# Kernel tuning notes

Measured on AMD Instinct MI355X. Metric: run time of the kernel, lower is better.

The kernel has to match this reference:

```python
import jax, jax.numpy as jnp
import numpy as np
from jax import lax

B_SZ, L, D, N = 4, 2048, 768, 16


def setup_inputs() -> dict:
    key = jax.random.key(0)
    ks = jax.random.split(key, 8)
    x = jax.random.normal(ks[0], (B_SZ, L, D), dtype=jnp.float32)
    # A_log init: log(repeat(arange(1, N+1), 'n -> d n'))
    A_log = jnp.log(jnp.tile(jnp.arange(1, N + 1, dtype=jnp.float32), (D, 1)))  # (D, N)
    sD = 1.0 / np.sqrt(D)
    Wb = jax.random.normal(ks[1], (N, D), dtype=jnp.float32) * sD
    bb = jax.random.normal(ks[2], (N,), dtype=jnp.float32) * sD
    Wc = jax.random.normal(ks[3], (N, D), dtype=jnp.float32) * sD
    bc = jax.random.normal(ks[4], (N,), dtype=jnp.float32) * sD
    W1 = jax.random.normal(ks[5], (1, D), dtype=jnp.float32) * sD
    b1 = jnp.zeros((1,), dtype=jnp.float32)
    Wd = jax.random.normal(ks[6], (D, 1), dtype=jnp.float32)
    bd = jax.random.normal(ks[7], (D,), dtype=jnp.float32)
    return {"x": x, "A_log": A_log, "Wb": Wb, "bb": bb, "Wc": Wc, "bc": bc,
            "W1": W1, "b1": b1, "Wd": Wd, "bd": bd}


def reference(x, A_log, Wb, bb, Wc, bc, W1, b1, Wd, bd):
    # x: (b, l, d)
    A = -jnp.exp(A_log)                                   # (d, n)
    Bp = x @ Wb.T + bb                                    # (b, l, n)
    C = x @ Wc.T + bc                                     # (b, l, n)
    s1 = x @ W1.T + b1                                    # (b, l, 1)
    delta = jax.nn.softplus(s1 @ Wd.T + bd)               # (b, l, d)
    deltaA = jnp.exp(jnp.einsum('bld,dn->bldn', delta, A))          # (b, l, d, n)
    deltaB_u = jnp.einsum('bld,bln,bld->bldn', delta, Bp, x)        # (b, l, d, n)

    def step(h, inputs):
        dA, dBu, c = inputs                               # (b,d,n),(b,d,n),(b,n)
        h = dA * h + dBu
        y = jnp.einsum('bdn,bn->bd', h, c)
        return h, y

    b, l, d = x.shape
    n = A_log.shape[1]
    h0 = jnp.zeros((b, d, n), dtype=x.dtype)
    _, ys = lax.scan(step, h0, (jnp.moveaxis(deltaA, 1, 0),
                                jnp.moveaxis(deltaB_u, 1, 0),
                                jnp.moveaxis(C, 1, 0)))
    return jnp.moveaxis(ys, 0, 1)                          # (b, l, d)
```

## Files before the change

kernel.cpp:

```cpp
#include <hip/hip_runtime.h>
#include <hip/hip_cooperative_groups.h>
#include <math.h>

namespace cg = cooperative_groups;

#define B_SZ 4
#define LSEQ 2048
#define DDIM 768
#define NST  16
#define NROW (B_SZ * LSEQ)
#define NJ   33

#define NC   64
#define CS   (LSEQ / NC)
#define CPG  (NC / 4)

#define KSPL 16
#define KCH  (DDIM / KSPL)

__global__ __launch_bounds__(256) void proj_part_kernel(
    const float* __restrict__ x,
    const float* __restrict__ Wb, const float* __restrict__ Wc,
    const float* __restrict__ W1, float* __restrict__ part)
{
    const int row = blockIdx.x * 256 + threadIdx.x;
    const int s = blockIdx.y;
    const int k0 = s * KCH;

    float4 xv[KCH / 4];
    const float* xp = x + (size_t)row * DDIM + k0;
    #pragma unroll
    for (int q = 0; q < KCH / 4; ++q) xv[q] = *(const float4*)(xp + q * 4);

    float acc[NJ];
    #pragma unroll
    for (int j = 0; j < NJ; ++j) {
        const float* wrow = (j < 16) ? (Wb + j * DDIM)
                          : (j < 32) ? (Wc + (j - 16) * DDIM)
                                     : W1;
        const float* wk = wrow + k0;
        float a = 0.f;
        #pragma unroll
        for (int q = 0; q < KCH / 4; ++q) {
            a = fmaf(xv[q].x, wk[q * 4 + 0], a);
            a = fmaf(xv[q].y, wk[q * 4 + 1], a);
            a = fmaf(xv[q].z, wk[q * 4 + 2], a);
            a = fmaf(xv[q].w, wk[q * 4 + 3], a);
        }
        acc[j] = a;
    }
    #pragma unroll
    for (int j = 0; j < NJ; ++j)
        part[((size_t)s * NJ + j) * NROW + row] = acc[j];
}

__global__ __launch_bounds__(256) void proj_reduce_kernel(
    const float* __restrict__ part,
    const float* __restrict__ bb, const float* __restrict__ bc,
    const float* __restrict__ b1,
    float* __restrict__ Bp, float* __restrict__ Cc, float* __restrict__ s1)
{
    const int idx = blockIdx.x * 256 + threadIdx.x;
    if (idx >= NJ * NROW) return;
    const int j = idx / NROW;
    const int row = idx % NROW;
    float a = 0.f;
    #pragma unroll
    for (int s = 0; s < KSPL; ++s)
        a += part[((size_t)s * NJ + j) * NROW + row];
    if (j < 16)      Bp[(size_t)row * NST + j] = a + bb[j];
    else if (j < 32) Cc[(size_t)row * NST + (j - 16)] = a + bc[j - 16];
    else             s1[row] = a + b1[0];
}

__device__ __forceinline__ float softplus_f(float z) {
    float t = __expf(-fabsf(z));
    return fmaxf(z, 0.f) + __logf(1.f + t);
}

__device__ __forceinline__ void powers16(float p, float* e) {
    e[0] = p;      e[1] = p * p;      e[2] = e[1] * p;   e[3] = e[1] * e[1];
    e[4] = e[3] * p;  e[5] = e[3] * e[1];  e[6] = e[3] * e[2];  e[7] = e[3] * e[3];
    e[8] = e[7] * p;  e[9] = e[7] * e[1];  e[10] = e[7] * e[2]; e[11] = e[7] * e[3];
    e[12] = e[7] * e[4]; e[13] = e[7] * e[5]; e[14] = e[7] * e[6]; e[15] = e[7] * e[7];
}

__device__ __forceinline__ bool a_structured(const float* acoef) {
    bool st = true;
    #pragma unroll
    for (int n = 0; n < NST; ++n)
        st = st && (fabsf(acoef[n] - (float)(n + 1) * acoef[0]) <= 1e-5f * fabsf(acoef[n]));
    return __all(st) != 0;
}

__device__ __forceinline__ void phaseA_body(
    int b, int c, int d,
    const float* __restrict__ x, const float* __restrict__ Wd, const float* __restrict__ bd,
    const float* __restrict__ Bp, const float* __restrict__ s1,
    const float* acoef, float a0, bool structured,
    float* __restrict__ Ssum, float* __restrict__ Q)
{
    const int rowbase = b * LSEQ + c * CS;
    const float wd = Wd[d], bdv = bd[d];
    const float4* B4 = (const float4*)(Bp + (size_t)rowbase * NST);
    const float* s1p = s1 + rowbase;
    const float* xp = x + (size_t)rowbase * DDIM + d;

    float h[NST];
    #pragma unroll
    for (int n = 0; n < NST; ++n) h[n] = 0.f;
    float S = 0.f;

    if (structured) {
        #pragma unroll 4
        for (int l = 0; l < CS; ++l) {
            const float delta = softplus_f(fmaf(s1p[l], wd, bdv));
            S += delta;
            float e[NST];
            powers16(__expf(delta * a0), e);
            const float dx = delta * xp[(size_t)l * DDIM];
            const float4 b0 = B4[l * 4 + 0], b1v = B4[l * 4 + 1];
            const float4 b2 = B4[l * 4 + 2], b3v = B4[l * 4 + 3];
            const float bv[NST] = {b0.x, b0.y, b0.z, b0.w, b1v.x, b1v.y, b1v.z, b1v.w,
                                   b2.x, b2.y, b2.z, b2.w, b3v.x, b3v.y, b3v.z, b3v.w};
            #pragma unroll
            for (int n = 0; n < NST; ++n) h[n] = fmaf(e[n], h[n], dx * bv[n]);
        }
    } else {
        #pragma unroll 4
        for (int l = 0; l < CS; ++l) {
            const float delta = softplus_f(fmaf(s1p[l], wd, bdv));
            S += delta;
            float e[NST];
            #pragma unroll
            for (int n = 0; n < NST; ++n) e[n] = __expf(delta * acoef[n]);
            const float dx = delta * xp[(size_t)l * DDIM];
            const float4 b0 = B4[l * 4 + 0], b1v = B4[l * 4 + 1];
            const float4 b2 = B4[l * 4 + 2], b3v = B4[l * 4 + 3];
            const float bv[NST] = {b0.x, b0.y, b0.z, b0.w, b1v.x, b1v.y, b1v.z, b1v.w,
                                   b2.x, b2.y, b2.z, b2.w, b3v.x, b3v.y, b3v.z, b3v.w};
            #pragma unroll
            for (int n = 0; n < NST; ++n) h[n] = fmaf(e[n], h[n], dx * bv[n]);
        }
    }
    Ssum[((size_t)b * NC + c) * DDIM + d] = S;
    const size_t gbase = (((size_t)b * NC + c) * DDIM + d) * NST;
    float4* Q4 = (float4*)(Q + gbase);
    #pragma unroll
    for (int q = 0; q < 4; ++q)
        Q4[q] = make_float4(h[q * 4], h[q * 4 + 1], h[q * 4 + 2], h[q * 4 + 3]);
}

__device__ __forceinline__ void phaseB_body(
    int gidx, int lane,
    const float* __restrict__ A_log,
    const float* __restrict__ Ssum, const float* __restrict__ Q,
    float* __restrict__ Hin)
{
    const int rlow = gidx & 15;
    const int g = (gidx >> 4) & 3;
    const int hi = gidx >> 6;
    const int pairIdx = hi * 16 + rlow;
    const int b2 = pairIdx / (DDIM * NST);
    const int r = pairIdx % (DDIM * NST);
    const int d2 = r >> 4;
    const float ac = -__expf(A_log[r]);
    const int c0 = g * CPG;

    float eq[CPG], qq[CPG];
    #pragma unroll
    for (int ci = 0; ci < CPG; ++ci) {
        const size_t base = (size_t)(b2 * NC + c0 + ci);
        eq[ci] = __expf(ac * Ssum[base * DDIM + d2]);
        qq[ci] = Q[base * (DDIM * NST) + r];
    }
    float E = 1.f, H = 0.f;
    #pragma unroll
    for (int ci = 0; ci < CPG; ++ci) { H = fmaf(eq[ci], H, qq[ci]); E *= eq[ci]; }

    float oE = __shfl_up(E, 16, 64);
    float oH = __shfl_up(H, 16, 64);
    if (lane >= 16) { H = fmaf(E, oH, H); E *= oE; }
    oE = __shfl_up(E, 32, 64);
    oH = __shfl_up(H, 32, 64);
    if (lane >= 32) { H = fmaf(E, oH, H); E *= oE; }

    float hin = __shfl_up(H, 16, 64);
    if (g == 0) hin = 0.f;

    float h = hin;
    #pragma unroll
    for (int ci = 0; ci < CPG; ++ci) {
        const size_t base = (size_t)(b2 * NC + c0 + ci);
        Hin[base * (DDIM * NST) + r] = h;
        h = fmaf(eq[ci], h, qq[ci]);
    }
}

__device__ __forceinline__ void phaseC_body(
    int b, int c, int d,
    const float* __restrict__ x, const float* __restrict__ Wd, const float* __restrict__ bd,
    const float* __restrict__ Bp, const float* __restrict__ Cc,
    const float* __restrict__ s1, const float* __restrict__ Hin,
    const float* acoef, float a0, bool structured,
    float* __restrict__ out)
{
    const int rowbase = b * LSEQ + c * CS;
    const float wd = Wd[d], bdv = bd[d];
    const float4* B4 = (const float4*)(Bp + (size_t)rowbase * NST);
    const float4* C4 = (const float4*)(Cc + (size_t)rowbase * NST);
    const float* s1p = s1 + rowbase;
    const float* xp = x + (size_t)rowbase * DDIM + d;
    float* yp = out + (size_t)rowbase * DDIM + d;

    float h[NST];
    const size_t gbase = (((size_t)b * NC + c) * DDIM + d) * NST;
    const float4* H4 = (const float4*)(Hin + gbase);
    #pragma unroll
    for (int q = 0; q < 4; ++q) {
        const float4 hv = H4[q];
        h[q * 4] = hv.x; h[q * 4 + 1] = hv.y; h[q * 4 + 2] = hv.z; h[q * 4 + 3] = hv.w;
    }

    if (structured) {
        #pragma unroll 4
        for (int l = 0; l < CS; ++l) {
            const float delta = softplus_f(fmaf(s1p[l], wd, bdv));
            float e[NST];
            powers16(__expf(delta * a0), e);
            const float dx = delta * xp[(size_t)l * DDIM];
            const float4 b0 = B4[l * 4 + 0], b1v = B4[l * 4 + 1];
            const float4 b2 = B4[l * 4 + 2], b3v = B4[l * 4 + 3];
            const float4 c0v = C4[l * 4 + 0], c1v = C4[l * 4 + 1];
            const float4 c2v = C4[l * 4 + 2], c3v = C4[l * 4 + 3];
            const float bv[NST] = {b0.x, b0.y, b0.z, b0.w, b1v.x, b1v.y, b1v.z, b1v.w,
                                   b2.x, b2.y, b2.z, b2.w, b3v.x, b3v.y, b3v.z, b3v.w};
            const float cv[NST] = {c0v.x, c0v.y, c0v.z, c0v.w, c1v.x, c1v.y, c1v.z, c1v.w,
                                   c2v.x, c2v.y, c2v.z, c2v.w, c3v.x, c3v.y, c3v.z, c3v.w};
            float y = 0.f;
            #pragma unroll
            for (int n = 0; n < NST; ++n) {
                h[n] = fmaf(e[n], h[n], dx * bv[n]);
                y = fmaf(h[n], cv[n], y);
            }
            yp[(size_t)l * DDIM] = y;
        }
    } else {
        #pragma unroll 4
        for (int l = 0; l < CS; ++l) {
            const float delta = softplus_f(fmaf(s1p[l], wd, bdv));
            float e[NST];
            #pragma unroll
            for (int n = 0; n < NST; ++n) e[n] = __expf(delta * acoef[n]);
            const float dx = delta * xp[(size_t)l * DDIM];
            const float4 b0 = B4[l * 4 + 0], b1v = B4[l * 4 + 1];
            const float4 b2 = B4[l * 4 + 2], b3v = B4[l * 4 + 3];
            const float4 c0v = C4[l * 4 + 0], c1v = C4[l * 4 + 1];
            const float4 c2v = C4[l * 4 + 2], c3v = C4[l * 4 + 3];
            const float bv[NST] = {b0.x, b0.y, b0.z, b0.w, b1v.x, b1v.y, b1v.z, b1v.w,
                                   b2.x, b2.y, b2.z, b2.w, b3v.x, b3v.y, b3v.z, b3v.w};
            const float cv[NST] = {c0v.x, c0v.y, c0v.z, c0v.w, c1v.x, c1v.y, c1v.z, c1v.w,
                                   c2v.x, c2v.y, c2v.z, c2v.w, c3v.x, c3v.y, c3v.z, c3v.w};
            float y = 0.f;
            #pragma unroll
            for (int n = 0; n < NST; ++n) {
                h[n] = fmaf(e[n], h[n], dx * bv[n]);
                y = fmaf(h[n], cv[n], y);
            }
            yp[(size_t)l * DDIM] = y;
        }
    }
}

__global__ __launch_bounds__(256) void pass1_kernel(
    const float* __restrict__ x, const float* __restrict__ A_log,
    const float* __restrict__ Wd, const float* __restrict__ bd,
    const float* __restrict__ Bp, const float* __restrict__ s1,
    float* __restrict__ Ssum, float* __restrict__ Q)
{
    const int d = blockIdx.x * 256 + threadIdx.x;
    const int c = blockIdx.y, b = blockIdx.z;
    float acoef[NST];
    #pragma unroll
    for (int n = 0; n < NST; ++n) acoef[n] = -__expf(A_log[d * NST + n]);
    const bool structured = a_structured(acoef);
    phaseA_body(b, c, d, x, Wd, bd, Bp, s1, acoef, acoef[0], structured, Ssum, Q);
}

__global__ __launch_bounds__(256) void combine_kernel(
    const float* __restrict__ A_log,
    const float* __restrict__ Ssum, const float* __restrict__ Q,
    float* __restrict__ Hin)
{
    const int gidx = blockIdx.x * 256 + threadIdx.x;
    phaseB_body(gidx, threadIdx.x & 63, A_log, Ssum, Q, Hin);
}

__global__ __launch_bounds__(256) void pass2_kernel(
    const float* __restrict__ x, const float* __restrict__ A_log,
    const float* __restrict__ Wd, const float* __restrict__ bd,
    const float* __restrict__ Bp, const float* __restrict__ Cc,
    const float* __restrict__ s1, const float* __restrict__ Hin,
    float* __restrict__ out)
{
    const int d = blockIdx.x * 256 + threadIdx.x;
    const int c = blockIdx.y, b = blockIdx.z;
    float acoef[NST];
    #pragma unroll
    for (int n = 0; n < NST; ++n) acoef[n] = -__expf(A_log[d * NST + n]);
    const bool structured = a_structured(acoef);
    phaseC_body(b, c, d, x, Wd, bd, Bp, Cc, s1, Hin, acoef, acoef[0], structured, out);
}

#define GRID_F (3 * B_SZ * NC)

__global__ __launch_bounds__(256, 3) void fused_scan_kernel(
    const float* __restrict__ x, const float* __restrict__ A_log,
    const float* __restrict__ Wd, const float* __restrict__ bd,
    const float* __restrict__ Bp, const float* __restrict__ Cc,
    const float* __restrict__ s1,
    float* __restrict__ Ssum, float* __restrict__ Q, float* __restrict__ Hin,
    float* __restrict__ out)
{
    const int tid = threadIdx.x;
    const int bx = blockIdx.x;
    const int dblk = bx / (B_SZ * NC);
    const int rem  = bx % (B_SZ * NC);
    const int b    = rem / NC;
    const int c    = rem % NC;
    const int d    = dblk * 256 + tid;

    float acoef[NST];
    #pragma unroll
    for (int n = 0; n < NST; ++n) acoef[n] = -__expf(A_log[d * NST + n]);
    const float a0 = acoef[0];
    const bool structured = a_structured(acoef);

    phaseA_body(b, c, d, x, Wd, bd, Bp, s1, acoef, a0, structured, Ssum, Q);

    __threadfence();
    cg::this_grid().sync();
    __threadfence();

    phaseB_body(bx * 256 + tid, tid & 63, A_log, Ssum, Q, Hin);

    __threadfence();
    cg::this_grid().sync();
    __threadfence();

    phaseC_body(b, c, d, x, Wd, bd, Bp, Cc, s1, Hin, acoef, a0, structured, out);
}

extern "C" void kernel_launch(void* const* d_in, const int* in_sizes, int n_in,
                              void* d_out, int out_size, void* d_ws, size_t ws_size,
                              hipStream_t stream) {
    const float* x     = (const float*)d_in[0];
    const float* A_log = (const float*)d_in[1];
    const float* Wb    = (const float*)d_in[2];
    const float* bb    = (const float*)d_in[3];
    const float* Wc    = (const float*)d_in[4];
    const float* bc    = (const float*)d_in[5];
    const float* W1    = (const float*)d_in[6];
    const float* b1    = (const float*)d_in[7];
    const float* Wd    = (const float*)d_in[8];
    const float* bd    = (const float*)d_in[9];
    float* out = (float*)d_out;

    float* ws = (float*)d_ws;
    const size_t partN = (size_t)KSPL * NJ * NROW;
    const size_t BpN = (size_t)NROW * NST;
    const size_t s1N = (size_t)NROW;
    const size_t sN  = (size_t)B_SZ * NC * DDIM;
    const size_t agg = (size_t)B_SZ * NC * DDIM * NST;

    float* part = ws;
    float* Bp   = part + partN;
    float* Cc   = Bp + BpN;
    float* s1   = Cc + BpN;
    float* Ssum = s1 + s1N;
    float* Q    = Ssum + sN;
    float* Hin  = Q + agg;

    dim3 gproj(NROW / 256, KSPL);
    proj_part_kernel<<<gproj, 256, 0, stream>>>(x, Wb, Wc, W1, part);
    proj_reduce_kernel<<<(NJ * NROW + 255) / 256, 256, 0, stream>>>(part, bb, bc, b1, Bp, Cc, s1);

    static int coop_mode = -1;
    if (coop_mode < 0) {
        int dev = 0;
        (void)hipGetDevice(&dev);
        int coopAttr = 0;
        (void)hipDeviceGetAttribute(&coopAttr, hipDeviceAttributeCooperativeLaunch, dev);
        int ncu = 0;
        (void)hipDeviceGetAttribute(&ncu, hipDeviceAttributeMultiprocessorCount, dev);
        int nblk = 0;
        hipError_t oe = hipOccupancyMaxActiveBlocksPerMultiprocessor(&nblk, fused_scan_kernel, 256, 0);
        coop_mode = (coopAttr && oe == hipSuccess && (long)nblk * ncu >= GRID_F) ? 1 : 0;
    }

    bool done = false;
    if (coop_mode == 1) {
        void* kargs[] = {(void*)&x, (void*)&A_log, (void*)&Wd, (void*)&bd,
                         (void*)&Bp, (void*)&Cc, (void*)&s1,
                         (void*)&Ssum, (void*)&Q, (void*)&Hin, (void*)&out};
        hipError_t le = hipLaunchCooperativeKernel((const void*)fused_scan_kernel,
                                                   dim3(GRID_F), dim3(256), kargs, 0, stream);
        if (le == hipSuccess) done = true;
        else coop_mode = 0;
    }
    if (!done) {
        dim3 gscan(DDIM / 256, NC, B_SZ);
        pass1_kernel<<<gscan, 256, 0, stream>>>(x, A_log, Wd, bd, Bp, s1, Ssum, Q);
        combine_kernel<<<(B_SZ * DDIM * NST * 4) / 256, 256, 0, stream>>>(A_log, Ssum, Q, Hin);
        pass2_kernel<<<gscan, 256, 0, stream>>>(x, A_log, Wd, bd, Bp, Cc, s1, Hin, out);
    }
}
```

Baseline: 157.0 us.

## Replace split-K projection with LDS-tiled single kernel and drop cooperative scan

The two-kernel split-K projection (partials written to workspace, then reduced) becomes one kernel. It stages 64-row tiles of x in double-buffered shared memory, and each wave computes 8 output columns, with wave 3 also computing the s1 projection. This removes the partial-sum round trip through global memory and one kernel launch. Separately, the cooperative fused scan kernel with grid syncs is removed and the three-kernel pass1/combine/pass2 path is always used, trading grid-barrier cost for two more launches. Weights are read directly from global memory per k, which may cost cache bandwidth.

```diff
diff --git a/kernel.cpp b/kernel.cpp
--- a/kernel.cpp
+++ b/kernel.cpp
@@ -1,76 +1,115 @@
 #include <hip/hip_runtime.h>
-#include <hip/hip_cooperative_groups.h>
 #include <math.h>
-
-namespace cg = cooperative_groups;
 
 #define B_SZ 4
 #define LSEQ 2048
 #define DDIM 768
 #define NST  16
 #define NROW (B_SZ * LSEQ)
-#define NJ   33
 
 #define NC   64
 #define CS   (LSEQ / NC)
 #define CPG  (NC / 4)
 
-#define KSPL 16
-#define KCH  (DDIM / KSPL)
-
-__global__ __launch_bounds__(256) void proj_part_kernel(
+#define RB   64
+#define KT   96
+#define NT   (DDIM / KT)
+#define LDSW (KT + 1)
+#define F4PT (RB * KT / 4 / 256)
+
+__global__ __launch_bounds__(256) void proj_kernel(
     const float* __restrict__ x,
     const float* __restrict__ Wb, const float* __restrict__ Wc,
-    const float* __restrict__ W1, float* __restrict__ part)
-{
-    const int row = blockIdx.x * 256 + threadIdx.x;
-    const int s = blockIdx.y;
-    const int k0 = s * KCH;
-
-    float4 xv[KCH / 4];
-    const float* xp = x + (size_t)row * DDIM + k0;
-    #pragma unroll
-    for (int q = 0; q < KCH / 4; ++q) xv[q] = *(const float4*)(xp + q * 4);
-
-    float acc[NJ];
-    #pragma unroll
-    for (int j = 0; j < NJ; ++j) {
-        const float* wrow = (j < 16) ? (Wb + j * DDIM)
-                          : (j < 32) ? (Wc + (j - 16) * DDIM)
-                                     : W1;
-        const float* wk = wrow + k0;
-        float a = 0.f;
-        #pragma unroll
-        for (int q = 0; q < KCH / 4; ++q) {
-            a = fmaf(xv[q].x, wk[q * 4 + 0], a);
-            a = fmaf(xv[q].y, wk[q * 4 + 1], a);
-            a = fmaf(xv[q].z, wk[q * 4 + 2], a);
-            a = fmaf(xv[q].w, wk[q * 4 + 3], a);
-        }
-        acc[j] = a;
-    }
-    #pragma unroll
-    for (int j = 0; j < NJ; ++j)
-        part[((size_t)s * NJ + j) * NROW + row] = acc[j];
-}
-
-__global__ __launch_bounds__(256) void proj_reduce_kernel(
-    const float* __restrict__ part,
+    const float* __restrict__ W1,
     const float* __restrict__ bb, const float* __restrict__ bc,
     const float* __restrict__ b1,
     float* __restrict__ Bp, float* __restrict__ Cc, float* __restrict__ s1)
 {
-    const int idx = blockIdx.x * 256 + threadIdx.x;
-    if (idx >= NJ * NROW) return;
-    const int j = idx / NROW;
-    const int row = idx % NROW;
-    float a = 0.f;
-    #pragma unroll
-    for (int s = 0; s < KSPL; ++s)
-        a += part[((size_t)s * NJ + j) * NROW + row];
-    if (j < 16)      Bp[(size_t)row * NST + j] = a + bb[j];
-    else if (j < 32) Cc[(size_t)row * NST + (j - 16)] = a + bc[j - 16];
-    else             s1[row] = a + b1[0];
+    __shared__ float xs[2][RB * LDSW];
+    const int tid = threadIdx.x;
+    const int row0 = blockIdx.x * RB;
+    const int w = tid >> 6;
+    const int l = tid & 63;
+
+    const float* wr[8];
+    #pragma unroll
+    for (int jj = 0; jj < 8; ++jj) {
+        const int j = w * 8 + jj;
+        wr[jj] = (j < 16) ? (Wb + j * DDIM) : (Wc + (j - 16) * DDIM);
+    }
+
+    float acc[8];
+    #pragma unroll
+    for (int jj = 0; jj < 8; ++jj) acc[jj] = 0.f;
+    float acc8 = 0.f;
+
+    const float4* x4 = (const float4*)x;
+    float4 g[F4PT];
+
+    #pragma unroll
+    for (int i = 0; i < F4PT; ++i) {
+        const int flat = i * 256 + tid;
+        const int rl = flat / (KT / 4), kk = flat % (KT / 4);
+        g[i] = x4[(size_t)(row0 + rl) * (DDIM / 4) + kk];
+    }
+    #pragma unroll
+    for (int i = 0; i < F4PT; ++i) {
+        const int flat = i * 256 + tid;
+        const int rl = flat / (KT / 4), kk = flat % (KT / 4);
+        float* p = &xs[0][rl * LDSW + kk * 4];
+        p[0] = g[i].x; p[1] = g[i].y; p[2] = g[i].z; p[3] = g[i].w;
+    }
+    __syncthreads();
+
+    for (int t = 0; t < NT; ++t) {
+        const int cur = t & 1;
+        if (t + 1 < NT) {
+            #pragma unroll
+            for (int i = 0; i < F4PT; ++i) {
+                const int flat = i * 256 + tid;
+                const int rl = flat / (KT / 4), kk = flat % (KT / 4);
+                g[i] = x4[(size_t)(row0 + rl) * (DDIM / 4) + (t + 1) * (KT / 4) + kk];
+            }
+        }
+        const int kg = t * KT;
+        const float* xrow = &xs[cur][l * LDSW];
+        #pragma unroll 4
+        for (int k = 0; k < KT; ++k) {
+            const float xv = xrow[k];
+            #pragma unroll
+            for (int jj = 0; jj < 8; ++jj)
+                acc[jj] = fmaf(xv, wr[jj][kg + k], acc[jj]);
+            if (w == 3) acc8 = fmaf(xv, W1[kg + k], acc8);
+        }
+        __syncthreads();
+        if (t + 1 < NT) {
+            #pragma unroll
+            for (int i = 0; i < F4PT; ++i) {
+                const int flat = i * 256 + tid;
+                const int rl = flat / (KT / 4), kk = flat % (KT / 4);
+                float* p = &xs[1 - cur][rl * LDSW + kk * 4];
+                p[0] = g[i].x; p[1] = g[i].y; p[2] = g[i].z; p[3] = g[i].w;
+            }
+            __syncthreads();
+        }
+    }
+
+    const int row = row0 + l;
+    if (w < 2) {
+        #pragma unroll
+        for (int jj = 0; jj < 8; ++jj) acc[jj] += bb[w * 8 + jj];
+        float4* o = (float4*)(Bp + (size_t)row * NST + w * 8);
+        o[0] = make_float4(acc[0], acc[1], acc[2], acc[3]);
+        o[1] = make_float4(acc[4], acc[5], acc[6], acc[7]);
+    } else {
+        const int jb = (w - 2) * 8;
+        #pragma unroll
+        for (int jj = 0; jj < 8; ++jj) acc[jj] += bc[jb + jj];
+        float4* o = (float4*)(Cc + (size_t)row * NST + jb);
+        o[0] = make_float4(acc[0], acc[1], acc[2], acc[3]);
+        o[1] = make_float4(acc[4], acc[5], acc[6], acc[7]);
+        if (w == 3) s1[row] = acc8 + b1[0];
+    }
 }
 
 __device__ __forceinline__ float softplus_f(float z) {
@@ -312,45 +351,6 @@
     phaseC_body(b, c, d, x, Wd, bd, Bp, Cc, s1, Hin, acoef, acoef[0], structured, out);
 }
 
-#define GRID_F (3 * B_SZ * NC)
-
-__global__ __launch_bounds__(256, 3) void fused_scan_kernel(
-    const float* __restrict__ x, const float* __restrict__ A_log,
-    const float* __restrict__ Wd, const float* __restrict__ bd,
-    const float* __restrict__ Bp, const float* __restrict__ Cc,
-    const float* __restrict__ s1,
-    float* __restrict__ Ssum, float* __restrict__ Q, float* __restrict__ Hin,
-    float* __restrict__ out)
-{
-    const int tid = threadIdx.x;
-    const int bx = blockIdx.x;
-    const int dblk = bx / (B_SZ * NC);
-    const int rem  = bx % (B_SZ * NC);
-    const int b    = rem / NC;
-    const int c    = rem % NC;
-    const int d    = dblk * 256 + tid;
-
-    float acoef[NST];
-    #pragma unroll
-    for (int n = 0; n < NST; ++n) acoef[n] = -__expf(A_log[d * NST + n]);
-    const float a0 = acoef[0];
-    const bool structured = a_structured(acoef);
-
-    phaseA_body(b, c, d, x, Wd, bd, Bp, s1, acoef, a0, structured, Ssum, Q);
-
-    __threadfence();
-    cg::this_grid().sync();
-    __threadfence();
-
-    phaseB_body(bx * 256 + tid, tid & 63, A_log, Ssum, Q, Hin);
-
-    __threadfence();
-    cg::this_grid().sync();
-    __threadfence();
-
-    phaseC_body(b, c, d, x, Wd, bd, Bp, Cc, s1, Hin, acoef, a0, structured, out);
-}
-
 extern "C" void kernel_launch(void* const* d_in, const int* in_sizes, int n_in,
                               void* d_out, int out_size, void* d_ws, size_t ws_size,
                               hipStream_t stream) {
@@ -367,51 +367,22 @@
     float* out = (float*)d_out;
 
     float* ws = (float*)d_ws;
-    const size_t partN = (size_t)KSPL * NJ * NROW;
     const size_t BpN = (size_t)NROW * NST;
     const size_t s1N = (size_t)NROW;
     const size_t sN  = (size_t)B_SZ * NC * DDIM;
     const size_t agg = (size_t)B_SZ * NC * DDIM * NST;
 
-    float* part = ws;
-    float* Bp   = part + partN;
+    float* Bp   = ws;
     float* Cc   = Bp + BpN;
     float* s1   = Cc + BpN;
     float* Ssum = s1 + s1N;
     float* Q    = Ssum + sN;
     float* Hin  = Q + agg;
 
-    dim3 gproj(NROW / 256, KSPL);
-    proj_part_kernel<<<gproj, 256, 0, stream>>>(x, Wb, Wc, W1, part);
-    proj_reduce_kernel<<<(NJ * NROW + 255) / 256, 256, 0, stream>>>(part, bb, bc, b1, Bp, Cc, s1);
-
-    static int coop_mode = -1;
-    if (coop_mode < 0) {
-        int dev = 0;
-        (void)hipGetDevice(&dev);
-        int coopAttr = 0;
-        (void)hipDeviceGetAttribute(&coopAttr, hipDeviceAttributeCooperativeLaunch, dev);
-        int ncu = 0;
-        (void)hipDeviceGetAttribute(&ncu, hipDeviceAttributeMultiprocessorCount, dev);
-        int nblk = 0;
-        hipError_t oe = hipOccupancyMaxActiveBlocksPerMultiprocessor(&nblk, fused_scan_kernel, 256, 0);
-        coop_mode = (coopAttr && oe == hipSuccess && (long)nblk * ncu >= GRID_F) ? 1 : 0;
-    }
-
-    bool done = false;
-    if (coop_mode == 1) {
-        void* kargs[] = {(void*)&x, (void*)&A_log, (void*)&Wd, (void*)&bd,
-                         (void*)&Bp, (void*)&Cc, (void*)&s1,
-                         (void*)&Ssum, (void*)&Q, (void*)&Hin, (void*)&out};
-        hipError_t le = hipLaunchCooperativeKernel((const void*)fused_scan_kernel,
-                                                   dim3(GRID_F), dim3(256), kargs, 0, stream);
-        if (le == hipSuccess) done = true;
-        else coop_mode = 0;
-    }
-    if (!done) {
-        dim3 gscan(DDIM / 256, NC, B_SZ);
-        pass1_kernel<<<gscan, 256, 0, stream>>>(x, A_log, Wd, bd, Bp, s1, Ssum, Q);
-        combine_kernel<<<(B_SZ * DDIM * NST * 4) / 256, 256, 0, stream>>>(A_log, Ssum, Q, Hin);
-        pass2_kernel<<<gscan, 256, 0, stream>>>(x, A_log, Wd, bd, Bp, Cc, s1, Hin, out);
-    }
-}
+    proj_kernel<<<NROW / RB, 256, 0, stream>>>(x, Wb, Wc, W1, bb, bc, b1, Bp, Cc, s1);
+
+    dim3 gscan(DDIM / 256, NC, B_SZ);
+    pass1_kernel<<<gscan, 256, 0, stream>>>(x, A_log, Wd, bd, Bp, s1, Ssum, Q);
+    combine_kernel<<<(B_SZ * DDIM * NST * 4) / 256, 256, 0, stream>>>(A_log, Ssum, Q, Hin);
+    pass2_kernel<<<gscan, 256, 0, stream>>>(x, A_log, Wd, bd, Bp, Cc, s1, Hin, out);
+}
```

After: 207.4 us. +32.1%, slower.
